# Kernel optimization log

Hardware: AMD Instinct MI355X
Metric: run time of the kernel (lower is better)

Reference implementation:

```python
import jax, jax.numpy as jnp
import numpy as np

B, C, H, W = 32, 512, 32, 32
HEADS = 8
HD = C // HEADS  # 64
BN_EPS = 1e-5


def setup_inputs() -> dict:
    key = jax.random.key(0)
    ks = jax.random.split(key, 8)
    s = 0.02  # trunc_normal std for Linear weights
    x = jax.random.normal(ks[0], (B, C, H, W), jnp.float32)
    Wq = jax.random.normal(ks[1], (C, C), jnp.float32) * s
    Wk = jax.random.normal(ks[2], (C, C), jnp.float32) * s
    Wv = jax.random.normal(ks[3], (C, C), jnp.float32) * s
    # depthwise 3x3 kernel, kaiming fan_out (fan_out = 3*3*1 per group)
    dw_w = jax.random.normal(ks[4], (C, 1, 3, 3), jnp.float32) * np.sqrt(2.0 / 9.0)
    bn_gamma = jnp.ones((C,), jnp.float32)
    bn_beta = jnp.zeros((C,), jnp.float32)
    temperature = jnp.ones((HEADS, 1, 1), jnp.float32)
    Wp = jax.random.normal(ks[5], (C, C), jnp.float32) * s
    bp = jnp.zeros((C,), jnp.float32)
    return {"x": x, "Wq": Wq, "Wk": Wk, "Wv": Wv, "dw_w": dw_w,
            "bn_gamma": bn_gamma, "bn_beta": bn_beta,
            "temperature": temperature, "Wp": Wp, "bp": bp}


def _l2norm(t):
    # torch F.normalize: x / max(||x||, eps)
    n = jnp.sqrt(jnp.sum(t * t, axis=-1, keepdims=True))
    return t / jnp.maximum(n, 1e-12)


def _forward(x, Wq, Wk, Wv, dw_w, bn_gamma, bn_beta, temperature, Wp, bp):
    b, c, h, w = x.shape
    n = h * w
    x_flat = x.transpose(0, 2, 3, 1).reshape(b, n, c)  # [B,N,C]

    q = (x_flat @ Wq.T).reshape(b, n, HEADS, HD).transpose(0, 2, 3, 1)  # [B,h,d,N]
    k = (x_flat @ Wk.T).reshape(b, n, HEADS, HD).transpose(0, 2, 3, 1)
    q = _l2norm(q)
    k = _l2norm(k)

    attn = jnp.einsum('bhdn,bhen->bhde', q, k) * temperature  # [B,h,d,d]
    attn = jax.nn.softmax(attn, axis=-1)

    v_content = x_flat @ Wv.T  # [B,N,C]

    # gated value path: DWConv -> BatchNorm (batch stats, train mode) -> SiLU
    g = jax.lax.conv_general_dilated(
        x, dw_w, window_strides=(1, 1), padding=((1, 1), (1, 1)),
        feature_group_count=c, dimension_numbers=('NCHW', 'OIHW', 'NCHW'))
    mu = jnp.mean(g, axis=(0, 2, 3), keepdims=True)
    var = jnp.var(g, axis=(0, 2, 3), keepdims=True)
    g = (g - mu) * jax.lax.rsqrt(var + BN_EPS)
    g = g * bn_gamma[None, :, None, None] + bn_beta[None, :, None, None]
    g = g * jax.nn.sigmoid(g)  # SiLU
    v_gate = g.transpose(0, 2, 3, 1).reshape(b, n, c)

    v = (v_content * v_gate).reshape(b, n, HEADS, HD).transpose(0, 2, 3, 1)  # [B,h,d,N]
    out = jnp.einsum('bhde,bhen->bhdn', attn, v)  # [B,h,d,N]
    out = out.transpose(0, 3, 1, 2).reshape(b, n, c)  # [B,N,C]
    out = out @ Wp.T + bp
    return out.reshape(b, h, w, c).transpose(0, 3, 1, 2)  # [B,C,H,W]


def reference(x, Wq, Wk, Wv, dw_w, bn_gamma, bn_beta, temperature, Wp, bp):
    return _forward(x, Wq, Wk, Wv, dw_w, bn_gamma, bn_beta, temperature, Wp, bp)
```

## Files before the change

### kernel.cpp

```cpp
#include <hip/hip_runtime.h>
#include <stdint.h>

#define BATCH 32
#define CCH   512
#define NPIX  1024
#define HEADS 8
#define QKV_M 1536

typedef short bf16x8 __attribute__((ext_vector_type(8)));
typedef float f32x4 __attribute__((ext_vector_type(4)));

__device__ inline float bf2f(unsigned short u) {
  union { float f; uint32_t i; } t; t.i = ((uint32_t)u) << 16; return t.f;
}
__device__ inline unsigned short f2bf(float f) {
  union { float f; uint32_t u; } t; t.f = f;
  uint32_t u = t.u;
  return (unsigned short)((u + 0x7FFFu + ((u >> 16) & 1u)) >> 16);
}

__device__ inline void gl_lds16(const unsigned short* g, unsigned short* l) {
  __builtin_amdgcn_global_load_lds(
      (const __attribute__((address_space(1))) uint32_t*)g,
      (__attribute__((address_space(3))) uint32_t*)l, 16, 0, 0);
}

__global__ void convert_w(const float* __restrict__ Wq, const float* __restrict__ Wk,
                          const float* __restrict__ Wv, const float* __restrict__ Wp,
                          unsigned short* __restrict__ wcat,
                          unsigned short* __restrict__ wpb) {
  int i = (blockIdx.x * 256 + threadIdx.x) * 4;
  union { ushort4 u4; unsigned short s[4]; } o;
  f32x4 a;
  a = *(const f32x4*)&Wq[i];
  for (int j = 0; j < 4; j++) o.s[j] = f2bf(a[j]);
  *(ushort4*)&wcat[i] = o.u4;
  a = *(const f32x4*)&Wk[i];
  for (int j = 0; j < 4; j++) o.s[j] = f2bf(a[j]);
  *(ushort4*)&wcat[CCH * CCH + i] = o.u4;
  a = *(const f32x4*)&Wv[i];
  for (int j = 0; j < 4; j++) o.s[j] = f2bf(a[j]);
  *(ushort4*)&wcat[2 * CCH * CCH + i] = o.u4;
  a = *(const f32x4*)&Wp[i];
  for (int j = 0; j < 4; j++) o.s[j] = f2bf(a[j]);
  *(ushort4*)&wpb[i] = o.u4;
}

__global__ void transpose_f2b(const float* __restrict__ in,
                              unsigned short* __restrict__ out, int R, int Cc) {
  __shared__ float tile[32][33];
  int b = blockIdx.z;
  int c0 = blockIdx.x * 32;
  int r0 = blockIdx.y * 32;
  const float* inb = in + (size_t)b * R * Cc;
  unsigned short* outb = out + (size_t)b * R * Cc;
  int tx = threadIdx.x, ty = threadIdx.y;
  for (int i = 0; i < 4; i++) {
    int r = ty + i * 8;
    tile[r][tx] = inb[(size_t)(r0 + r) * Cc + c0 + tx];
  }
  __syncthreads();
  for (int i = 0; i < 4; i++) {
    int r = ty + i * 8;
    outb[(size_t)(c0 + r) * R + r0 + tx] = f2bf(tile[tx][r]);
  }
}

template <bool OUT_F32>
__launch_bounds__(256)
__global__ void gemm_bt(const unsigned short* __restrict__ A,
                        const unsigned short* __restrict__ X,
                        void* __restrict__ Cout,
                        const float* __restrict__ bias,
                        int M, int N, int K) {
  __shared__ __align__(16) unsigned short As[128 * 64];
  __shared__ __align__(16) unsigned short Bs[128 * 64];
  int b  = blockIdx.z;
  int m0 = blockIdx.y * 128;
  int n0 = blockIdx.x * 128;
  const unsigned short* Xb = X + (size_t)b * N * K;
  int tid = threadIdx.x;
  int lane = tid & 63;
  int wave = tid >> 6;
  int wm = wave >> 1, wn = wave & 1;
  int quad = lane >> 4, l16 = lane & 15;

  f32x4 acc[4][4];
  f32x4 zero = {0.f, 0.f, 0.f, 0.f};
  for (int i = 0; i < 4; i++)
    for (int j = 0; j < 4; j++) acc[i][j] = zero;

  int r8 = lane >> 3;
  int sw = ((lane & 7) ^ r8) * 8;
  const unsigned short* Ag = A  + (size_t)(m0 + wave * 32 + r8) * K + sw;
  const unsigned short* Xg = Xb + (size_t)(n0 + wave * 32 + r8) * K + sw;
  unsigned short* Al = &As[wave * 32 * 64];
  unsigned short* Bl = &Bs[wave * 32 * 64];

  for (int k0 = 0; k0 < K; k0 += 64) {
    for (int i = 0; i < 4; i++) {
      gl_lds16(Ag + k0 + i * 8 * K, Al + i * 8 * 64);
      gl_lds16(Xg + k0 + i * 8 * K, Bl + i * 8 * 64);
    }
    __syncthreads();
    bf16x8 af[2][4], bfr[2][4];
    for (int ks = 0; ks < 2; ks++)
      for (int i = 0; i < 4; i++) {
        int ch = ((ks * 4 + quad) ^ (l16 & 7)) * 8;
        af[ks][i]  = *(const bf16x8*)&As[(wm * 64 + i * 16 + l16) * 64 + ch];
        bfr[ks][i] = *(const bf16x8*)&Bs[(wn * 64 + i * 16 + l16) * 64 + ch];
      }
    for (int ks = 0; ks < 2; ks++)
      for (int i = 0; i < 4; i++)
        for (int j = 0; j < 4; j++)
          acc[i][j] = __builtin_amdgcn_mfma_f32_16x16x32_bf16(
              af[ks][i], bfr[ks][j], acc[i][j], 0, 0, 0);
    __syncthreads();
  }

  for (int i = 0; i < 4; i++) {
    int gmb = m0 + wm * 64 + i * 16 + quad * 4;
    for (int j = 0; j < 4; j++) {
      int gn = n0 + wn * 64 + j * 16 + l16;
      for (int r = 0; r < 4; r++) {
        int gm = gmb + r;
        float v = acc[i][j][r];
        if (OUT_F32) {
          v += bias[gm];
          ((float*)Cout)[(size_t)b * M * N + (size_t)gm * N + gn] = v;
        } else {
          ((unsigned short*)Cout)[(size_t)b * M * N + (size_t)gm * N + gn] = f2bf(v);
        }
      }
    }
  }
}

__global__ void dw_stats(const float* __restrict__ x,
                         const float* __restrict__ wgt,
                         float* __restrict__ s1, float* __restrict__ s2) {
  int c = blockIdx.x, b = blockIdx.y;
  __shared__ __align__(16) float plane[NPIX];
  const float* xp = x + ((size_t)b * CCH + c) * NPIX;
  *(f32x4*)&plane[threadIdx.x * 4] = *(const f32x4*)&xp[threadIdx.x * 4];
  __syncthreads();
  float w[9];
  for (int i = 0; i < 9; i++) w[i] = wgt[c * 9 + i];
  float a1 = 0.f, a2 = 0.f;
  for (int pi = 0; pi < 4; pi++) {
    int p = threadIdx.x + pi * 256;
    int h = p >> 5, wc = p & 31;
    float v = 0.f;
    for (int dh = -1; dh <= 1; dh++)
      for (int dw = -1; dw <= 1; dw++) {
        int hh = h + dh, ww = wc + dw;
        if (hh >= 0 && hh < 32 && ww >= 0 && ww < 32)
          v += w[(dh + 1) * 3 + dw + 1] * plane[hh * 32 + ww];
      }
    a1 += v; a2 += v * v;
  }
  for (int off = 32; off > 0; off >>= 1) {
    a1 += __shfl_down(a1, off);
    a2 += __shfl_down(a2, off);
  }
  __shared__ float r1[4], r2[4];
  int wv = threadIdx.x >> 6;
  if ((threadIdx.x & 63) == 0) { r1[wv] = a1; r2[wv] = a2; }
  __syncthreads();
  if (threadIdx.x == 0) {
    atomicAdd(&s1[c], r1[0] + r1[1] + r1[2] + r1[3]);
    atomicAdd(&s2[c], r2[0] + r2[1] + r2[2] + r2[3]);
  }
}

__global__ void gate_apply(const float* __restrict__ x,
                           const float* __restrict__ wgt,
                           const float* __restrict__ s1, const float* __restrict__ s2,
                           const float* __restrict__ gamma,
                           const float* __restrict__ beta,
                           unsigned short* __restrict__ qkv) {
  int c = blockIdx.x, b = blockIdx.y;
  __shared__ __align__(16) float plane[NPIX];
  const float* xp = x + ((size_t)b * CCH + c) * NPIX;
  unsigned short* vp = qkv + ((size_t)b * QKV_M + 2 * CCH + c) * NPIX;
  *(f32x4*)&plane[threadIdx.x * 4] = *(const f32x4*)&xp[threadIdx.x * 4];
  __syncthreads();
  float w[9];
  for (int i = 0; i < 9; i++) w[i] = wgt[c * 9 + i];
  const float invn = 1.f / 32768.f;
  float mean = s1[c] * invn;
  float var = fmaxf(s2[c] * invn - mean * mean, 0.f);
  float rstd = rsqrtf(var + 1e-5f);
  float ga = gamma[c], be = beta[c];
  for (int pi = 0; pi < 4; pi++) {
    int p = threadIdx.x + pi * 256;
    int h = p >> 5, wc = p & 31;
    float val = 0.f;
    for (int dh = -1; dh <= 1; dh++)
      for (int dw = -1; dw <= 1; dw++) {
        int hh = h + dh, ww = wc + dw;
        if (hh >= 0 && hh < 32 && ww >= 0 && ww < 32)
          val += w[(dh + 1) * 3 + dw + 1] * plane[hh * 32 + ww];
      }
    float g = (val - mean) * rstd * ga + be;
    float sg = g / (1.f + __expf(-g));
    vp[p] = f2bf(bf2f(vp[p]) * sg);
  }
}

__launch_bounds__(256)
__global__ void attn_s(const unsigned short* __restrict__ qkv,
                       const float* __restrict__ temp,
                       unsigned short* __restrict__ P) {
  int bh = blockIdx.x;
  int b = bh >> 3, h = bh & 7;
  const unsigned short* Q = qkv + ((size_t)b * QKV_M + h * 64) * NPIX;
  const unsigned short* K = Q + (size_t)CCH * NPIX;
  int tid = threadIdx.x, lane = tid & 63, wave = tid >> 6;
  int quad = lane >> 4, l16 = lane & 15;

  __shared__ __align__(16) float Sf[64][65];
  __shared__ float qq[64], kk[64], invq[64], invk[64];
  __shared__ float redm[4][64], reds[4][64];

  f32x4 zero = {0.f, 0.f, 0.f, 0.f};
  f32x4 acc[4], accQ = zero, accK = zero;
  for (int j = 0; j < 4; j++) acc[j] = zero;
  for (int n0 = 0; n0 < NPIX; n0 += 32) {
    bf16x8 a  = *(const bf16x8*)&Q[(size_t)(wave * 16 + l16) * NPIX + n0 + quad * 8];
    bf16x8 ak = *(const bf16x8*)&K[(size_t)(wave * 16 + l16) * NPIX + n0 + quad * 8];
    accQ = __builtin_amdgcn_mfma_f32_16x16x32_bf16(a, a, accQ, 0, 0, 0);
    accK = __builtin_amdgcn_mfma_f32_16x16x32_bf16(ak, ak, accK, 0, 0, 0);
    for (int j = 0; j < 4; j++) {
      bf16x8 bb = *(const bf16x8*)&K[(size_t)(j * 16 + l16) * NPIX + n0 + quad * 8];
      acc[j] = __builtin_amdgcn_mfma_f32_16x16x32_bf16(a, bb, acc[j], 0, 0, 0);
    }
  }
  for (int j = 0; j < 4; j++)
    for (int r = 0; r < 4; r++)
      Sf[wave * 16 + quad * 4 + r][j * 16 + l16] = acc[j][r];
  for (int r = 0; r < 4; r++)
    if (l16 == quad * 4 + r) {
      qq[wave * 16 + l16] = accQ[r];
      kk[wave * 16 + l16] = accK[r];
    }
  __syncthreads();
  if (tid < 64) invq[tid] = 1.f / fmaxf(sqrtf(qq[tid]), 1e-12f);
  else if (tid < 128) invk[tid - 64] = 1.f / fmaxf(sqrtf(kk[tid - 64]), 1e-12f);
  __syncthreads();

  int row = tid & 63, seg = tid >> 6;
  float fq = temp[h] * invq[row];
  float v[16], pm = -1e30f;
  for (int i = 0; i < 16; i++) {
    v[i] = Sf[row][seg * 16 + i] * fq * invk[seg * 16 + i];
    pm = fmaxf(pm, v[i]);
  }
  redm[seg][row] = pm;
  __syncthreads();
  float m = fmaxf(fmaxf(redm[0][row], redm[1][row]),
                  fmaxf(redm[2][row], redm[3][row]));
  float ps = 0.f;
  for (int i = 0; i < 16; i++) { v[i] = __expf(v[i] - m); ps += v[i]; }
  reds[seg][row] = ps;
  __syncthreads();
  float inv = 1.f / (reds[0][row] + reds[1][row] + reds[2][row] + reds[3][row]);
  union { uint4 q4[2]; unsigned short s[16]; } u;
  for (int i = 0; i < 16; i++) u.s[i] = f2bf(v[i] * inv);
  unsigned short* Pp = P + ((size_t)bh * 64 + row) * 64 + seg * 16;
  *(uint4*)&Pp[0] = u.q4[0];
  *(uint4*)&Pp[8] = u.q4[1];
}

__launch_bounds__(256)
__global__ void attn_o(const unsigned short* __restrict__ qkv,
                       const unsigned short* __restrict__ P,
                       unsigned short* __restrict__ aoT) {
  int blk = blockIdx.x;
  int nc = blk & 3, bh = blk >> 2;
  int b = bh >> 3, h = bh & 7;
  const unsigned short* V = qkv + ((size_t)b * QKV_M + 2 * CCH + h * 64) * NPIX;
  unsigned short* Ob = aoT + (size_t)b * NPIX * CCH + h * 64;
  int tid = threadIdx.x, lane = tid & 63, wave = tid >> 6;
  int quad = lane >> 4, l16 = lane & 15;

  __shared__ __align__(16) unsigned short Vt[4][16][72];
  __shared__ __align__(16) unsigned short Ot[4][16][72];

  const unsigned short* Pb = P + (size_t)bh * 64 * 64;
  bf16x8 Pf[4][2];
  for (int j = 0; j < 4; j++)
    for (int ks = 0; ks < 2; ks++)
      Pf[j][ks] = *(const bf16x8*)&Pb[(j * 16 + l16) * 64 + ks * 32 + quad * 8];

  f32x4 zero = {0.f, 0.f, 0.f, 0.f};
  int e1 = lane >> 1, noff = (lane & 1) * 8;
  int nbase = nc * 256 + wave * 64;
  int orow = lane >> 3, ocol = (lane & 7) * 8;

  union { uint4 q; unsigned short s[8]; } g0, g1, c0, c1;
  g0.q = *(const uint4*)&V[(size_t)e1 * NPIX + nbase + noff];
  g1.q = *(const uint4*)&V[(size_t)(e1 + 32) * NPIX + nbase + noff];
#pragma unroll
  for (int nt = 0; nt < 4; nt++) {
    int n0 = nbase + nt * 16;
    c0 = g0; c1 = g1;
    if (nt < 3) {
      g0.q = *(const uint4*)&V[(size_t)e1 * NPIX + n0 + 16 + noff];
      g1.q = *(const uint4*)&V[(size_t)(e1 + 32) * NPIX + n0 + 16 + noff];
    }
    for (int jj = 0; jj < 8; jj++) {
      Vt[wave][noff + jj][e1]      = c0.s[jj];
      Vt[wave][noff + jj][e1 + 32] = c1.s[jj];
    }
    bf16x8 Af0 = *(const bf16x8*)&Vt[wave][l16][quad * 8];
    bf16x8 Af1 = *(const bf16x8*)&Vt[wave][l16][32 + quad * 8];
    f32x4 oacc[4];
    for (int j = 0; j < 4; j++) {
      oacc[j] = __builtin_amdgcn_mfma_f32_16x16x32_bf16(Af0, Pf[j][0], zero, 0, 0, 0);
      oacc[j] = __builtin_amdgcn_mfma_f32_16x16x32_bf16(Af1, Pf[j][1], oacc[j], 0, 0, 0);
    }
    for (int j = 0; j < 4; j++)
      for (int r = 0; r < 4; r++)
        Ot[wave][quad * 4 + r][j * 16 + l16] = f2bf(oacc[j][r]);
    uint4 o0 = *(const uint4*)&Ot[wave][orow][ocol];
    uint4 o1 = *(const uint4*)&Ot[wave][orow + 8][ocol];
    *(uint4*)&Ob[(size_t)(n0 + orow) * CCH + ocol] = o0;
    *(uint4*)&Ob[(size_t)(n0 + orow + 8) * CCH + ocol] = o1;
  }
}

extern "C" void kernel_launch(void* const* d_in, const int* in_sizes, int n_in,
                              void* d_out, int out_size, void* d_ws, size_t ws_size,
                              hipStream_t stream) {
  const float* x     = (const float*)d_in[0];
  const float* Wq    = (const float*)d_in[1];
  const float* Wk    = (const float*)d_in[2];
  const float* Wv    = (const float*)d_in[3];
  const float* dww   = (const float*)d_in[4];
  const float* gamma = (const float*)d_in[5];
  const float* beta  = (const float*)d_in[6];
  const float* temp  = (const float*)d_in[7];
  const float* Wp    = (const float*)d_in[8];
  const float* bp    = (const float*)d_in[9];
  float* out = (float*)d_out;

  char* ws = (char*)d_ws;
  unsigned short* wcat = (unsigned short*)ws;
  unsigned short* wpb  = wcat + (size_t)QKV_M * CCH;
  float* s1 = (float*)(wpb + (size_t)CCH * CCH);
  float* s2 = s1 + CCH;
  unsigned short* Pbuf = (unsigned short*)(s2 + CCH);
  char* dyn = (char*)(Pbuf + (size_t)BATCH * HEADS * 64 * 64);
  size_t fixed = (size_t)(dyn - ws);
  size_t per_b = ((size_t)NPIX * CCH + (size_t)QKV_M * NPIX) * 2;
  int BC = BATCH;
  while (BC > 1 && fixed + (size_t)BC * per_b > ws_size) BC >>= 1;
  unsigned short* xT  = (unsigned short*)dyn;
  unsigned short* qkv = xT + (size_t)BC * NPIX * CCH;

  convert_w<<<CCH * CCH / 1024, 256, 0, stream>>>(Wq, Wk, Wv, Wp, wcat, wpb);
  hipMemsetAsync(s1, 0, 2 * CCH * sizeof(float), stream);
  dw_stats<<<dim3(CCH, BATCH), 256, 0, stream>>>(x, dww, s1, s2);

  for (int b0 = 0; b0 < BATCH; b0 += BC) {
    const float* xc = x + (size_t)b0 * CCH * NPIX;
    float* outc = out + (size_t)b0 * CCH * NPIX;
    transpose_f2b<<<dim3(NPIX / 32, CCH / 32, BC), dim3(32, 8), 0, stream>>>(
        xc, xT, CCH, NPIX);
    gemm_bt<false><<<dim3(NPIX / 128, QKV_M / 128, BC), 256, 0, stream>>>(
        wcat, xT, qkv, nullptr, QKV_M, NPIX, CCH);
    attn_s<<<BC * HEADS, 256, 0, stream>>>(qkv, temp, Pbuf);
    gate_apply<<<dim3(CCH, BC), 256, 0, stream>>>(xc, dww, s1, s2, gamma, beta, qkv);
    attn_o<<<BC * HEADS * 4, 256, 0, stream>>>(qkv, Pbuf, xT);
    gemm_bt<true><<<dim3(NPIX / 128, CCH / 128, BC), 256, 0, stream>>>(
        wpb, xT, outc, bp, CCH, NPIX, CCH);
  }
}
```

Before: 333.0 us.

## Enlarge GEMM tiles to 256x256 with 8 waves and double-buffered LDS pipeline

Rewrites the bf16 MFMA GEMM to use 256x256 block tiles with 512 threads. Global-to-LDS loads now go through a double buffer, so the next K tile is fetched while the current one is computed. Compute is split into four phases with explicit waitcnt, barriers and setprio to interleave LDS reads with MFMA. This raises data reuse and hides load latency, but it uses 128KB of LDS and more registers per block, and it leaves fewer blocks to fill the device (e.g. the projection GEMM gets 4x2x32 blocks).

```diff
diff --git a/kernel.cpp b/kernel.cpp
--- a/kernel.cpp
+++ b/kernel.cpp
@@ -67,70 +67,118 @@
 }
 
 template <bool OUT_F32>
-__launch_bounds__(256)
+__launch_bounds__(512, 2)
 __global__ void gemm_bt(const unsigned short* __restrict__ A,
                         const unsigned short* __restrict__ X,
                         void* __restrict__ Cout,
                         const float* __restrict__ bias,
                         int M, int N, int K) {
-  __shared__ __align__(16) unsigned short As[128 * 64];
-  __shared__ __align__(16) unsigned short Bs[128 * 64];
-  int b  = blockIdx.z;
-  int m0 = blockIdx.y * 128;
-  int n0 = blockIdx.x * 128;
+  __shared__ __align__(16) unsigned short As[2][256 * 64];
+  __shared__ __align__(16) unsigned short Bs[2][256 * 64];
+  const int b  = blockIdx.z;
+  const int m0 = blockIdx.y * 256;
+  const int n0 = blockIdx.x * 256;
   const unsigned short* Xb = X + (size_t)b * N * K;
-  int tid = threadIdx.x;
-  int lane = tid & 63;
-  int wave = tid >> 6;
-  int wm = wave >> 1, wn = wave & 1;
-  int quad = lane >> 4, l16 = lane & 15;
-
-  f32x4 acc[4][4];
-  f32x4 zero = {0.f, 0.f, 0.f, 0.f};
-  for (int i = 0; i < 4; i++)
+  const int tid  = threadIdx.x;
+  const int lane = tid & 63;
+  const int wave = tid >> 6;
+  const int wm = wave >> 2;
+  const int wn = wave & 3;
+  const int quad = lane >> 4, l16 = lane & 15;
+
+  f32x4 acc[8][4];
+  const f32x4 zero = {0.f, 0.f, 0.f, 0.f};
+#pragma unroll
+  for (int i = 0; i < 8; i++)
+#pragma unroll
     for (int j = 0; j < 4; j++) acc[i][j] = zero;
 
-  int r8 = lane >> 3;
-  int sw = ((lane & 7) ^ r8) * 8;
-  const unsigned short* Ag = A  + (size_t)(m0 + wave * 32 + r8) * K + sw;
-  const unsigned short* Xg = Xb + (size_t)(n0 + wave * 32 + r8) * K + sw;
-  unsigned short* Al = &As[wave * 32 * 64];
-  unsigned short* Bl = &Bs[wave * 32 * 64];
-
-  for (int k0 = 0; k0 < K; k0 += 64) {
-    for (int i = 0; i < 4; i++) {
-      gl_lds16(Ag + k0 + i * 8 * K, Al + i * 8 * 64);
-      gl_lds16(Xg + k0 + i * 8 * K, Bl + i * 8 * 64);
-    }
-    __syncthreads();
-    bf16x8 af[2][4], bfr[2][4];
-    for (int ks = 0; ks < 2; ks++)
-      for (int i = 0; i < 4; i++) {
-        int ch = ((ks * 4 + quad) ^ (l16 & 7)) * 8;
-        af[ks][i]  = *(const bf16x8*)&As[(wm * 64 + i * 16 + l16) * 64 + ch];
-        bfr[ks][i] = *(const bf16x8*)&Bs[(wn * 64 + i * 16 + l16) * 64 + ch];
-      }
-    for (int ks = 0; ks < 2; ks++)
-      for (int i = 0; i < 4; i++)
-        for (int j = 0; j < 4; j++)
-          acc[i][j] = __builtin_amdgcn_mfma_f32_16x16x32_bf16(
-              af[ks][i], bfr[ks][j], acc[i][j], 0, 0, 0);
-    __syncthreads();
-  }
-
-  for (int i = 0; i < 4; i++) {
-    int gmb = m0 + wm * 64 + i * 16 + quad * 4;
-    for (int j = 0; j < 4; j++) {
-      int gn = n0 + wn * 64 + j * 16 + l16;
-      for (int r = 0; r < 4; r++) {
-        int gm = gmb + r;
-        float v = acc[i][j][r];
-        if (OUT_F32) {
-          v += bias[gm];
-          ((float*)Cout)[(size_t)b * M * N + (size_t)gm * N + gn] = v;
-        } else {
-          ((unsigned short*)Cout)[(size_t)b * M * N + (size_t)gm * N + gn] = f2bf(v);
+  const int r8  = lane >> 3;
+  const int swk = ((lane & 7) ^ r8) * 8;
+  const unsigned short* Ag = A  + (size_t)(m0 + wave * 32 + r8) * K + swk;
+  const unsigned short* Xg = Xb + (size_t)(n0 + wave * 32 + r8) * K + swk;
+
+  const int NT = K >> 6;
+
+  auto stage = [&](int kt, int bsel) {
+    unsigned short* Al = &As[bsel][wave * 32 * 64];
+    unsigned short* Bl = &Bs[bsel][wave * 32 * 64];
+    const unsigned short* Agk = Ag + kt * 64;
+    const unsigned short* Xgk = Xg + kt * 64;
+#pragma unroll
+    for (int i = 0; i < 4; ++i) {
+      gl_lds16(Agk + (size_t)i * 8 * K, Al + i * 8 * 64);
+      gl_lds16(Xgk + (size_t)i * 8 * K, Bl + i * 8 * 64);
+    }
+  };
+
+  stage(0, 0);
+  for (int t = 0; t < NT; ++t) {
+    const int cur = t & 1;
+    if (t + 1 < NT) {
+      stage(t + 1, cur ^ 1);
+      asm volatile("s_waitcnt vmcnt(8)" ::: "memory");
+    } else {
+      asm volatile("s_waitcnt vmcnt(0)" ::: "memory");
+    }
+    __builtin_amdgcn_s_barrier();
+    const unsigned short* Asl = As[cur];
+    const unsigned short* Bsl = Bs[cur];
+#pragma unroll
+    for (int ph = 0; ph < 4; ++ph) {
+      const int Qm = ph >> 1, Qn = ph & 1;
+      bf16x8 af[4][2], bfr[2][2];
+#pragma unroll
+      for (int ii = 0; ii < 4; ++ii)
+#pragma unroll
+        for (int ks = 0; ks < 2; ++ks) {
+          const int row = wm * 128 + (Qm * 4 + ii) * 16 + l16;
+          const int ch  = ((ks * 4 + quad) ^ (l16 & 7)) * 8;
+          af[ii][ks] = *(const bf16x8*)&Asl[row * 64 + ch];
         }
+#pragma unroll
+      for (int jj = 0; jj < 2; ++jj)
+#pragma unroll
+        for (int ks = 0; ks < 2; ++ks) {
+          const int row = wn * 64 + (Qn * 2 + jj) * 16 + l16;
+          const int ch  = ((ks * 4 + quad) ^ (l16 & 7)) * 8;
+          bfr[jj][ks] = *(const bf16x8*)&Bsl[row * 64 + ch];
+        }
+      __builtin_amdgcn_s_barrier();
+      asm volatile("s_waitcnt lgkmcnt(0)" ::: "memory");
+      __builtin_amdgcn_sched_barrier(0);
+      __builtin_amdgcn_s_setprio(1);
+#pragma unroll
+      for (int ks = 0; ks < 2; ++ks)
+#pragma unroll
+        for (int ii = 0; ii < 4; ++ii)
+#pragma unroll
+          for (int jj = 0; jj < 2; ++jj)
+            acc[Qm * 4 + ii][Qn * 2 + jj] =
+                __builtin_amdgcn_mfma_f32_16x16x32_bf16(
+                    af[ii][ks], bfr[jj][ks],
+                    acc[Qm * 4 + ii][Qn * 2 + jj], 0, 0, 0);
+      __builtin_amdgcn_s_setprio(0);
+      __builtin_amdgcn_s_barrier();
+    }
+  }
+
+#pragma unroll
+  for (int i = 0; i < 8; ++i) {
+#pragma unroll
+    for (int r = 0; r < 4; ++r) {
+      const int gm = m0 + wm * 128 + i * 16 + quad * 4 + r;
+      if constexpr (OUT_F32) {
+        const float bv = bias[gm];
+        float* Co = (float*)Cout + (size_t)b * M * N + (size_t)gm * N +
+                    n0 + wn * 64 + l16;
+#pragma unroll
+        for (int j = 0; j < 4; ++j) Co[j * 16] = acc[i][j][r] + bv;
+      } else {
+        unsigned short* Co = (unsigned short*)Cout + (size_t)b * M * N +
+                             (size_t)gm * N + n0 + wn * 64 + l16;
+#pragma unroll
+        for (int j = 0; j < 4; ++j) Co[j * 16] = f2bf(acc[i][j][r]);
       }
     }
   }
@@ -368,12 +416,12 @@
     float* outc = out + (size_t)b0 * CCH * NPIX;
     transpose_f2b<<<dim3(NPIX / 32, CCH / 32, BC), dim3(32, 8), 0, stream>>>(
         xc, xT, CCH, NPIX);
-    gemm_bt<false><<<dim3(NPIX / 128, QKV_M / 128, BC), 256, 0, stream>>>(
+    gemm_bt<false><<<dim3(NPIX / 256, QKV_M / 256, BC), 512, 0, stream>>>(
         wcat, xT, qkv, nullptr, QKV_M, NPIX, CCH);
     attn_s<<<BC * HEADS, 256, 0, stream>>>(qkv, temp, Pbuf);
     gate_apply<<<dim3(CCH, BC), 256, 0, stream>>>(xc, dww, s1, s2, gamma, beta, qkv);
     attn_o<<<BC * HEADS * 4, 256, 0, stream>>>(qkv, Pbuf, xT);
-    gemm_bt<true><<<dim3(NPIX / 128, CCH / 128, BC), 256, 0, stream>>>(
+    gemm_bt<true><<<dim3(NPIX / 256, CCH / 256, BC), 512, 0, stream>>>(
         wpb, xT, outc, bp, CCH, NPIX, CCH);
   }
 }
```

New measurement: 343.6 us. +3.2%, slower.
